# Kernel optimization log

Hardware: AMD Instinct MI355X
Metric: run time of the kernel (lower is better)

The kernel has to match this reference:

```python
import jax, jax.numpy as jnp
import numpy as np
import math

B, S, HID, H, WBAND = 2, 4096, 768, 12, 128
D = HID // H  # 64


def _band_qk(q, k, w):
    """q,k: [B,S,H,D] -> banded scores [B,S,H,2w+1] (offset d -> key pos i+d-w)."""
    b, s, h, d = q.shape
    nc = s // w
    kp = jnp.pad(k, ((0, 0), (w, w), (0, 0), (0, 0)))  # zero padding_value
    idx = (jnp.arange(nc) * w)[:, None] + jnp.arange(3 * w)[None, :]  # [nc,3w]
    kw = kp[:, idx]                                   # [B,nc,3w,H,D]
    qc = q.reshape(b, nc, w, h, d)
    scores = jnp.einsum('bcxhd,bcyhd->bchxy', qc, kw)  # [B,nc,H,w,3w]
    # extract diagonals: P[x,dd] = scores[x, x+dd] via flatten/skew trick
    flat = scores.reshape(b, nc, h, w * 3 * w)
    flat = jnp.pad(flat, ((0, 0), (0, 0), (0, 0), (0, w)))
    diag = flat.reshape(b, nc, h, w, 3 * w + 1)[..., : 2 * w + 1]
    return diag.transpose(0, 1, 3, 2, 4).reshape(b, s, h, 2 * w + 1)


def _band_pv(p, v, w):
    """p: [B,S,H,2w+1], v: [B,S,H,D] -> context [B,S,H,D]."""
    b, s, h, k = p.shape
    d = v.shape[-1]
    nc = s // w
    vp = jnp.pad(v, ((0, 0), (w, w), (0, 0), (0, 0)))
    idx = (jnp.arange(nc) * w)[:, None] + jnp.arange(3 * w)[None, :]
    vw = vp[:, idx]                                   # [B,nc,3w,H,D]
    pc = p.reshape(b, nc, w, h, k).transpose(0, 1, 3, 2, 4)  # [B,nc,H,w,2w+1]
    pc = jnp.pad(pc, ((0, 0), (0, 0), (0, 0), (0, 0), (0, w)))  # [..,w,3w+1]
    band = pc.reshape(b, nc, h, w * (3 * w + 1))[..., : w * 3 * w]
    band = band.reshape(b, nc, h, w, 3 * w)           # M[x, x+dd] = p[x,dd]
    ctx = jnp.einsum('bchxy,bcyhd->bcxhd', band, vw)  # [B,nc,w,H,D]
    return ctx.reshape(b, s, h, d)


def setup_inputs() -> dict:
    key = jax.random.key(0)
    ks = jax.random.split(key, 8)
    init = lambda k, shp: (jax.random.normal(k, shp, jnp.float32) * 0.02)
    return {
        'x': jax.random.normal(ks[0], (B, S, HID), jnp.float32),
        'Wq': init(ks[1], (HID, HID)), 'bq': jnp.zeros((HID,), jnp.float32),
        'Wk': init(ks[2], (HID, HID)), 'bk': jnp.zeros((HID,), jnp.float32),
        'Wv': init(ks[3], (HID, HID)), 'bv': jnp.zeros((HID,), jnp.float32),
        'Wd': init(ks[4], (H, D, HID)), 'bd': jnp.zeros((HID,), jnp.float32),
        'gamma': jnp.ones((HID,), jnp.float32),
        'beta': jnp.zeros((HID,), jnp.float32),
    }


def reference(x, Wq, bq, Wk, bk, Wv, bv, Wd, bd, gamma, beta):
    w = WBAND
    b, s, _ = x.shape
    q = (x @ Wq + bq).reshape(b, s, H, D) / math.sqrt(D)
    k = (x @ Wk + bk).reshape(b, s, H, D)
    v = (x @ Wv + bv).reshape(b, s, H, D)
    scores = _band_qk(q, k, w)                        # [B,S,H,2w+1]
    # mask_invalid_locations: key pos i + d - w must lie in [0, S)
    pos = jnp.arange(s)[:, None] + jnp.arange(2 * w + 1)[None, :] - w
    valid = (pos >= 0) & (pos < s)                    # [S,2w+1]
    scores = jnp.where(valid[None, :, None, :], scores, -1e9)
    probs = jax.nn.softmax(scores, axis=-1)           # float32 softmax
    ctx = _band_pv(probs, v, w)                       # [B,S,H,D]
    proj = jnp.einsum('bfnd,ndh->bfh', ctx, Wd) + bd  # output projection
    y = x + proj                                      # residual (dropout=0)
    mu = jnp.mean(y, axis=-1, keepdims=True)
    var = jnp.mean(jnp.square(y - mu), axis=-1, keepdims=True)
    out = (y - mu) / jnp.sqrt(var + 1e-12) * gamma + beta
    return out
```

## Files before the change

### kernel.cpp

```cpp
#include <hip/hip_runtime.h>
#include <math.h>

typedef unsigned short u16;
typedef __bf16 bf16x8 __attribute__((ext_vector_type(8)));
typedef float f32x4 __attribute__((ext_vector_type(4)));

constexpr int Bc   = 2;
constexpr int Sc   = 4096;
constexpr int HIDc = 768;
constexpr int Hc   = 12;
constexpr int Dc   = 64;
constexpr int Wc   = 128;
constexpr int Mc   = Bc * Sc;

constexpr int QT2  = 64;
constexpr int WIN  = QT2 + 2 * Wc;
constexpr int NCT  = WIN / 16;

#define VM_BAR(N) asm volatile("s_waitcnt vmcnt(" #N ")\n\ts_barrier" ::: "memory")
#define BAR()     asm volatile("s_barrier" ::: "memory")

static __device__ __forceinline__ void load_lds16(const void* g, void* l) {
    __builtin_amdgcn_global_load_lds(
        (const __attribute__((address_space(1))) void*)g,
        (__attribute__((address_space(3))) void*)l, 16, 0, 0);
}
static __device__ __forceinline__ u16 to_bf16(float f) {
    return __builtin_bit_cast(u16, (__bf16)f);
}

__global__ __launch_bounds__(256) void prep_x(const float* __restrict__ x,
                                              u16* __restrict__ xb,
                                              u16* __restrict__ zpad)
{
    int i = blockIdx.x * 256 + threadIdx.x;
    float4 v = ((const float4*)x)[i];
    ushort4 o;
    o.x = to_bf16(v.x); o.y = to_bf16(v.y);
    o.z = to_bf16(v.z); o.w = to_bf16(v.w);
    ((ushort4*)xb)[i] = o;
    if (blockIdx.x == 0 && threadIdx.x < 128)
        ((int4*)zpad)[threadIdx.x] = make_int4(0, 0, 0, 0);
}

__global__ __launch_bounds__(256) void prep_w(
    const float* __restrict__ Wq, const float* __restrict__ Wk,
    const float* __restrict__ Wv, const float* __restrict__ Wd,
    u16* __restrict__ wqt, u16* __restrict__ wkt,
    u16* __restrict__ wvt, u16* __restrict__ wdt)
{
    const int z = blockIdx.z;
    const float* W = z == 0 ? Wq : z == 1 ? Wk : z == 2 ? Wv : Wd;
    u16* T         = z == 0 ? wqt : z == 1 ? wkt : z == 2 ? wvt : wdt;

    __shared__ float t[32][33];
    const int bx = blockIdx.x * 32, by = blockIdx.y * 32;
    const int tx = threadIdx.x & 31, ty = threadIdx.x >> 5;
#pragma unroll
    for (int i = 0; i < 32; i += 8)
        t[ty + i][tx] = W[(size_t)(by + ty + i) * HIDc + bx + tx];
    __syncthreads();
#pragma unroll
    for (int i = 0; i < 32; i += 8)
        T[(size_t)(bx + ty + i) * HIDc + by + tx] = to_bf16(t[tx][ty + i]);
}

__device__ __forceinline__ void stage64(const u16* __restrict__ A,
                                        const u16* __restrict__ Bt,
                                        int m0, int n0, int k0,
                                        u16* As, u16* Bs, int soff)
{
#pragma unroll
    for (int i = 0; i < 4; ++i) {
        int off  = soff + i * 1024;
        int row  = off >> 7;
        int slot = (off >> 4) & 7;
        int seg  = slot ^ (row & 7);
        load_lds16(A  + (size_t)(m0 + row) * HIDc + k0 + seg * 8, (char*)As + off);
        load_lds16(Bt + (size_t)(n0 + row) * HIDc + k0 + seg * 8, (char*)Bs + off);
    }
}

template <int SWAP>
__device__ __forceinline__ void gemm128_core(
    const u16* __restrict__ A, const u16* __restrict__ Bt,
    int m0, int n0, u16* As, u16* Bs, f32x4 (&acc)[4][4])
{
    const int lane = threadIdx.x & 63, wid = threadIdx.x >> 6;
    const int c16 = lane & 15, g = lane >> 4;
    const int wm = (wid >> 1) * 64, wn = (wid & 1) * 64;
    const int soff = wid * 4096 + lane * 16;

    stage64(A, Bt, m0, n0, 0, As, Bs, soff);
    int cur = 0;
    for (int t = 0; t < 12; ++t) {
        if (t < 11) {
            stage64(A, Bt, m0, n0, (t + 1) * 64,
                    As + (cur ^ 1) * 8192, Bs + (cur ^ 1) * 8192, soff);
            VM_BAR(8);
        } else {
            VM_BAR(0);
        }
        const u16* Ab = As + cur * 8192;
        const u16* Bb = Bs + cur * 8192;
#pragma unroll
        for (int kk = 0; kk < 2; ++kk) {
            bf16x8 af[4], bfr[4];
#pragma unroll
            for (int tt = 0; tt < 4; ++tt) {
                int ar = wm + tt * 16 + c16;
                int a8 = (kk * 4 + g) ^ (ar & 7);
                af[tt] = *(const bf16x8*)(Ab + ar * 64 + a8 * 8);
                int br = wn + tt * 16 + c16;
                int b8 = (kk * 4 + g) ^ (br & 7);
                bfr[tt] = *(const bf16x8*)(Bb + br * 64 + b8 * 8);
            }
            __builtin_amdgcn_s_setprio(1);
#pragma unroll
            for (int mt = 0; mt < 4; ++mt)
#pragma unroll
                for (int nt = 0; nt < 4; ++nt)
                    acc[mt][nt] = SWAP
                        ? __builtin_amdgcn_mfma_f32_16x16x32_bf16(
                              bfr[nt], af[mt], acc[mt][nt], 0, 0, 0)
                        : __builtin_amdgcn_mfma_f32_16x16x32_bf16(
                              af[mt], bfr[nt], acc[mt][nt], 0, 0, 0);
            __builtin_amdgcn_s_setprio(0);
        }
        BAR();
        cur ^= 1;
    }
}

__global__ __launch_bounds__(256) void gemm_qk_mfma(
    const u16* __restrict__ xb,
    const u16* __restrict__ wqt, const u16* __restrict__ wkt,
    const float* __restrict__ bq, const float* __restrict__ bk,
    u16* __restrict__ qg, u16* __restrict__ kg)
{
    __shared__ u16 As[16384], Bs[16384];
    const int z = blockIdx.z;
    const u16* Bt     = z ? wkt : wqt;
    const float* bias = z ? bk : bq;
    const float scale = z ? 1.0f : 0.125f;
    u16* outp         = z ? kg : qg;

    const int m0 = blockIdx.x * 128, n0 = blockIdx.y * 128;
    f32x4 acc[4][4];
#pragma unroll
    for (int i = 0; i < 4; ++i)
#pragma unroll
        for (int j = 0; j < 4; ++j) acc[i][j] = (f32x4){0.f, 0.f, 0.f, 0.f};

    gemm128_core<1>(xb, Bt, m0, n0, As, Bs, acc);

    const int lane = threadIdx.x & 63, wid = threadIdx.x >> 6;
    const int c16 = lane & 15, g = lane >> 4;
    const int wm = (wid >> 1) * 64, wn = (wid & 1) * 64;

#pragma unroll
    for (int mt = 0; mt < 4; ++mt) {
        int m = m0 + wm + mt * 16 + c16;
        int b = m >> 12, s = m & (Sc - 1);
        size_t rowbase = (size_t)(b * Hc) * Sc * Dc + (size_t)s * Dc;
#pragma unroll
        for (int nt = 0; nt < 4; ++nt) {
            int nb = n0 + wn + nt * 16 + g * 4;
            int h = nb >> 6, d0 = nb & 63;
            float4 b4 = *(const float4*)&bias[nb];
            ushort4 pk;
            pk.x = to_bf16((acc[mt][nt][0] + b4.x) * scale);
            pk.y = to_bf16((acc[mt][nt][1] + b4.y) * scale);
            pk.z = to_bf16((acc[mt][nt][2] + b4.z) * scale);
            pk.w = to_bf16((acc[mt][nt][3] + b4.w) * scale);
            *(ushort4*)&outp[rowbase + (size_t)h * Sc * Dc + d0] = pk;
        }
    }
}

__global__ __launch_bounds__(256) void gemm_v_mfma(
    const u16* __restrict__ xb, const u16* __restrict__ wvt,
    const float* __restrict__ bv, u16* __restrict__ vtg)
{
    __shared__ u16 As[16384], Bs[16384];
    const int m0 = blockIdx.x * 128, n0 = blockIdx.y * 128;
    f32x4 acc[4][4];
#pragma unroll
    for (int i = 0; i < 4; ++i)
#pragma unroll
        for (int j = 0; j < 4; ++j) acc[i][j] = (f32x4){0.f, 0.f, 0.f, 0.f};

    gemm128_core<0>(xb, wvt, m0, n0, As, Bs, acc);

    const int lane = threadIdx.x & 63, wid = threadIdx.x >> 6;
    const int c16 = lane & 15, g = lane >> 4;
    const int wm = (wid >> 1) * 64, wn = (wid & 1) * 64;

#pragma unroll
    for (int nt = 0; nt < 4; ++nt) {
        int n = n0 + wn + nt * 16 + c16;
        int h = n >> 6, d = n & 63;
        float bn = bv[n];
#pragma unroll
        for (int mt = 0; mt < 4; ++mt) {
            int m = m0 + wm + mt * 16 + g * 4;
            int b = m >> 12, s = m & (Sc - 1);
            size_t base = ((size_t)(b * Hc + h)) * Sc * Dc + (size_t)d * Sc + s;
            ushort4 pk;
            pk.x = to_bf16(acc[mt][nt][0] + bn);
            pk.y = to_bf16(acc[mt][nt][1] + bn);
            pk.z = to_bf16(acc[mt][nt][2] + bn);
            pk.w = to_bf16(acc[mt][nt][3] + bn);
            *(ushort4*)&vtg[base] = pk;
        }
    }
}

__global__ __launch_bounds__(256) void gemm_proj_mfma(
    const u16* __restrict__ ctxb, const u16* __restrict__ wdt,
    const float* __restrict__ bd, const float* __restrict__ x,
    float* __restrict__ y)
{
    __shared__ u16 As[16384], Bs[16384];
    const int m0 = blockIdx.x * 128, n0 = blockIdx.y * 128;
    f32x4 acc[4][4];
#pragma unroll
    for (int i = 0; i < 4; ++i)
#pragma unroll
        for (int j = 0; j < 4; ++j) acc[i][j] = (f32x4){0.f, 0.f, 0.f, 0.f};

    gemm128_core<1>(ctxb, wdt, m0, n0, As, Bs, acc);

    const int lane = threadIdx.x & 63, wid = threadIdx.x >> 6;
    const int c16 = lane & 15, g = lane >> 4;
    const int wm = (wid >> 1) * 64, wn = (wid & 1) * 64;

#pragma unroll
    for (int mt = 0; mt < 4; ++mt) {
        int m = m0 + wm + mt * 16 + c16;
#pragma unroll
        for (int nt = 0; nt < 4; ++nt) {
            int nb = n0 + wn + nt * 16 + g * 4;
            float4 b4 = *(const float4*)&bd[nb];
            float4 x4 = *(const float4*)&x[(size_t)m * HIDc + nb];
            float4 o4;
            o4.x = acc[mt][nt][0] + b4.x + x4.x;
            o4.y = acc[mt][nt][1] + b4.y + x4.y;
            o4.z = acc[mt][nt][2] + b4.z + x4.z;
            o4.w = acc[mt][nt][3] + b4.w + x4.w;
            *(float4*)&y[(size_t)m * HIDc + nb] = o4;
        }
    }
}

__global__ __launch_bounds__(256) void band_attn_mfma(
    const u16* __restrict__ qg, const u16* __restrict__ kg,
    const u16* __restrict__ vtg, const u16* __restrict__ zpad,
    u16* __restrict__ ctxb)
{
    extern __shared__ u16 sm[];
    u16* kwin = sm;
    u16* vt   = sm + 20480;
    u16* pm   = sm;

    const int L = blockIdx.x;
    const int xcd = L & 7, tt = L >> 3;
    const int hb = xcd * 3 + (tt % 3);
    const int qc = tt / 3;
    const int h = hb % Hc, b = hb / Hc;

    const int s0 = qc * QT2;
    const int tid = threadIdx.x;
    const int lane = tid & 63, wid = tid >> 6;
    const int c16 = lane & 15, g = lane >> 4;
    const size_t hbase = ((size_t)(b * Hc + h)) * Sc * Dc;

    const u16* qp = &qg[hbase + (size_t)(s0 + wid * 16 + c16) * Dc + g * 8];
    bf16x8 qa0 = *(const bf16x8*)qp;
    bf16x8 qa1 = *(const bf16x8*)(qp + 32);

#pragma unroll
    for (int i = 0; i < 10; ++i) {
        int c   = i * 4 + wid;
        int row = c * 8 + (lane >> 3);
        int seg = (lane & 7) ^ (lane >> 3);
        int pos = s0 - Wc + row;
        const u16* src = (pos >= 0 && pos < Sc)
                       ? &kg[hbase + (size_t)pos * Dc + seg * 8] : zpad;
        load_lds16(src, (char*)kwin + c * 1024 + (lane & 63) * 16);
    }
#pragma unroll
    for (int i = 0; i < 10; ++i) {
        int c   = i * 4 + wid;
        int idx = c * 64 + lane;
        int d   = idx / 40;
        int p   = idx - d * 40;
        int seg = (p & 0x38) | ((p ^ d) & 7);
        int pos0 = s0 - Wc + seg * 8;
        const u16* src = (pos0 >= 0 && pos0 < Sc)
                       ? &vtg[hbase + (size_t)d * Sc + pos0] : zpad;
        load_lds16(src, (char*)vt + idx * 16);
    }

    VM_BAR(10);

    f32x4 acc[NCT];
#pragma unroll
    for (int ct = 0; ct < NCT; ++ct) acc[ct] = (f32x4){0.f, 0.f, 0.f, 0.f};
    __builtin_amdgcn_s_setprio(1);
#pragma unroll
    for (int ct = 0; ct < NCT; ++ct) {
        int row = ct * 16 + c16;
        const u16* kb = kwin + row * 64;
        bf16x8 kb0 = *(const bf16x8*)(kb + (g       ^ (row & 7)) * 8);
        bf16x8 kb1 = *(const bf16x8*)(kb + ((g + 4) ^ (row & 7)) * 8);
        acc[ct] = __builtin_amdgcn_mfma_f32_16x16x32_bf16(qa0, kb0, acc[ct], 0, 0, 0);
        acc[ct] = __builtin_amdgcn_mfma_f32_16x16x32_bf16(qa1, kb1, acc[ct], 0, 0, 0);
    }
    __builtin_amdgcn_s_setprio(0);

    float mrow[4] = {-3e38f, -3e38f, -3e38f, -3e38f};
#pragma unroll
    for (int ct = 0; ct < NCT; ++ct) {
#pragma unroll
        for (int r = 0; r < 4; ++r) {
            int rl  = wid * 16 + g * 4 + r;
            int j   = ct * 16 + c16;
            int pos = s0 - Wc + j;
            bool valid = (j >= rl) && (j <= rl + 2 * Wc) && (pos >= 0) && (pos < Sc);
            float v = valid ? acc[ct][r] : -3e38f;
            acc[ct][r] = v;
            mrow[r] = fmaxf(mrow[r], v);
        }
    }
#pragma unroll
    for (int r = 0; r < 4; ++r)
#pragma unroll
        for (int off = 1; off < 16; off <<= 1)
            mrow[r] = fmaxf(mrow[r], __shfl_xor(mrow[r], off));

    float srow[4] = {0.f, 0.f, 0.f, 0.f};
#pragma unroll
    for (int ct = 0; ct < NCT; ++ct)
#pragma unroll
        for (int r = 0; r < 4; ++r) {
            float e = __expf(acc[ct][r] - mrow[r]);
            acc[ct][r] = e;
            srow[r] += e;
        }
#pragma unroll
    for (int r = 0; r < 4; ++r)
#pragma unroll
        for (int off = 1; off < 16; off <<= 1)
            srow[r] += __shfl_xor(srow[r], off);

    VM_BAR(0);

#pragma unroll
    for (int ct = 0; ct < NCT; ++ct)
#pragma unroll
        for (int r = 0; r < 4; ++r) {
            int q   = wid * 16 + g * 4 + r;
            int col = ct * 16 + c16;
            int sl  = col >> 3;
            int ph  = (sl & 0x38) | ((sl ^ q ^ (q >> 3)) & 7);
            pm[q * 320 + ph * 8 + (col & 7)] = to_bf16(acc[ct][r]);
        }

    float sq0 = __shfl(srow[0], (c16 >> 2) << 4);
    float sq1 = __shfl(srow[1], (c16 >> 2) << 4);
    float sq2 = __shfl(srow[2], (c16 >> 2) << 4);
    float sq3 = __shfl(srow[3], (c16 >> 2) << 4);
    int rr = c16 & 3;
    float sq = rr == 0 ? sq0 : rr == 1 ? sq1 : rr == 2 ? sq2 : sq3;
    float invq = 1.f / sq;

    f32x4 o[4];
#pragma unroll
    for (int dt = 0; dt < 4; ++dt) o[dt] = (f32x4){0.f, 0.f, 0.f, 0.f};
    const int qrow = wid * 16 + c16;
    __builtin_amdgcn_s_setprio(1);
#pragma unroll
    for (int ks = 0; ks < 10; ++ks) {
        int sl = ks * 4 + g;
        int ph = (sl & 0x38) | ((sl ^ qrow ^ (qrow >> 3)) & 7);
        bf16x8 pa = *(const bf16x8*)(pm + qrow * 320 + ph * 8);
#pragma unroll
        for (int dt = 0; dt < 4; ++dt) {
            int d  = dt * 16 + c16;
            int pv = (sl & 0x38) | ((sl ^ d) & 7);
            bf16x8 vb = *(const bf16x8*)(vt + d * 320 + pv * 8);
            o[dt] = __builtin_amdgcn_mfma_f32_16x16x32_bf16(vb, pa, o[dt], 0, 0, 0);
        }
    }
    __builtin_amdgcn_s_setprio(0);

    const size_t crow = ((size_t)(b * Sc + s0 + wid * 16 + c16)) * HIDc + h * Dc;
#pragma unroll
    for (int dt = 0; dt < 4; ++dt) {
        ushort4 pk;
        pk.x = to_bf16(o[dt][0] * invq);
        pk.y = to_bf16(o[dt][1] * invq);
        pk.z = to_bf16(o[dt][2] * invq);
        pk.w = to_bf16(o[dt][3] * invq);
        *(ushort4*)&ctxb[crow + dt * 16 + g * 4] = pk;
    }
}

__global__ __launch_bounds__(256) void ln_kernel(
    const float* __restrict__ y,
    const float* __restrict__ gamma, const float* __restrict__ beta,
    float* __restrict__ out)
{
    const int m = blockIdx.x;
    const float* row = y + (size_t)m * HIDc;
    const int t = threadIdx.x;
    float v0 = row[t], v1 = row[t + 256], v2 = row[t + 512];
    float s = v0 + v1 + v2;
    __shared__ float red[4];
    const int lane = t & 63, wid = t >> 6;
#pragma unroll
    for (int o = 1; o < 64; o <<= 1) s += __shfl_xor(s, o);
    if (lane == 0) red[wid] = s;
    __syncthreads();
    const float mu = (red[0] + red[1] + red[2] + red[3]) * (1.f / HIDc);
    v0 -= mu; v1 -= mu; v2 -= mu;
    float s2 = v0 * v0 + v1 * v1 + v2 * v2;
#pragma unroll
    for (int o = 1; o < 64; o <<= 1) s2 += __shfl_xor(s2, o);
    __syncthreads();
    if (lane == 0) red[wid] = s2;
    __syncthreads();
    const float var = (red[0] + red[1] + red[2] + red[3]) * (1.f / HIDc);
    const float rstd = rsqrtf(var + 1e-12f);
    const size_t base = (size_t)m * HIDc;
    out[base + t]       = v0 * rstd * gamma[t]       + beta[t];
    out[base + t + 256] = v1 * rstd * gamma[t + 256] + beta[t + 256];
    out[base + t + 512] = v2 * rstd * gamma[t + 512] + beta[t + 512];
}

extern "C" void kernel_launch(void* const* d_in, const int* in_sizes, int n_in,
                              void* d_out, int out_size, void* d_ws, size_t ws_size,
                              hipStream_t stream)
{
    const float* x     = (const float*)d_in[0];
    const float* Wq    = (const float*)d_in[1];
    const float* bq    = (const float*)d_in[2];
    const float* Wk    = (const float*)d_in[3];
    const float* bk    = (const float*)d_in[4];
    const float* Wv    = (const float*)d_in[5];
    const float* bv    = (const float*)d_in[6];
    const float* Wd    = (const float*)d_in[7];
    const float* bd    = (const float*)d_in[8];
    const float* gamma = (const float*)d_in[9];
    const float* beta  = (const float*)d_in[10];
    float* out = (float*)d_out;

    constexpr size_t CHUNK = (size_t)Mc * HIDc;
    constexpr size_t WSZ   = (size_t)HIDc * HIDc;
    u16* xb   = (u16*)d_ws;
    u16* wqt  = xb + CHUNK;
    u16* wkt  = wqt + WSZ;
    u16* wvt  = wkt + WSZ;
    u16* wdt  = wvt + WSZ;
    u16* qg   = wdt + WSZ;
    u16* kg   = qg + CHUNK;
    u16* vtg  = kg + CHUNK;
    u16* ctxb = vtg + CHUNK;
    float* yws = (float*)(ctxb + CHUNK);
    u16* zpad  = (u16*)(yws + CHUNK);

    prep_x<<<(CHUNK / 4) / 256, 256, 0, stream>>>(x, xb, zpad);
    prep_w<<<dim3(24, 24, 4), 256, 0, stream>>>(Wq, Wk, Wv, Wd, wqt, wkt, wvt, wdt);

    gemm_qk_mfma<<<dim3(Mc / 128, HIDc / 128, 2), 256, 0, stream>>>(
        xb, wqt, wkt, bq, bk, qg, kg);
    gemm_v_mfma<<<dim3(Mc / 128, HIDc / 128), 256, 0, stream>>>(
        xb, wvt, bv, vtg);

    band_attn_mfma<<<dim3(Sc / QT2 * Hc * Bc), 256, 81920, stream>>>(
        qg, kg, vtg, zpad, ctxb);

    gemm_proj_mfma<<<dim3(Mc / 128, HIDc / 128), 256, 0, stream>>>(
        ctxb, wdt, bd, x, yws);

    ln_kernel<<<Mc, 256, 0, stream>>>(yws, gamma, beta, out);
}
```

Measured before the change: 126.7 us.

## Widen band attention to 128-query tiles with per-wave diagonal key windows

The band-attention kernel now runs 512-thread blocks over 128 queries. The K/V window grows to 384 keys, so loaded K/V is shared by twice as many queries and there are half as many blocks. Each wave computes only the 18 key tiles its 16 rows can reach rather than the whole window, which cuts wasted QK and PV MFMA work on masked entries. The probability staging buffer shrinks to 192 columns and is filled and consumed in two halves. The cost is larger LDS use per block (96 KB), more registers per wave and fewer blocks, which may lower occupancy.

```diff
diff --git a/kernel.cpp b/kernel.cpp
--- a/kernel.cpp
+++ b/kernel.cpp
@@ -13,9 +13,9 @@
 constexpr int Wc   = 128;
 constexpr int Mc   = Bc * Sc;
 
-constexpr int QT2  = 64;
-constexpr int WIN  = QT2 + 2 * Wc;
-constexpr int NCT  = WIN / 16;
+constexpr int QT3  = 128;
+constexpr int WIN3 = 384;
+constexpr int NCT3 = 18;
 
 #define VM_BAR(N) asm volatile("s_waitcnt vmcnt(" #N ")\n\ts_barrier" ::: "memory")
 #define BAR()     asm volatile("s_barrier" ::: "memory")
@@ -253,14 +253,14 @@
     }
 }
 
-__global__ __launch_bounds__(256) void band_attn_mfma(
+__global__ __launch_bounds__(512) void band_attn_mfma(
     const u16* __restrict__ qg, const u16* __restrict__ kg,
     const u16* __restrict__ vtg, const u16* __restrict__ zpad,
     u16* __restrict__ ctxb)
 {
     extern __shared__ u16 sm[];
     u16* kwin = sm;
-    u16* vt   = sm + 20480;
+    u16* vt   = sm + 24576;
     u16* pm   = sm;
 
     const int L = blockIdx.x;
@@ -269,19 +269,19 @@
     const int qc = tt / 3;
     const int h = hb % Hc, b = hb / Hc;
 
-    const int s0 = qc * QT2;
+    const int s0 = qc * QT3;
     const int tid = threadIdx.x;
-    const int lane = tid & 63, wid = tid >> 6;
+    const int lane = tid & 63, w = tid >> 6;
     const int c16 = lane & 15, g = lane >> 4;
     const size_t hbase = ((size_t)(b * Hc + h)) * Sc * Dc;
 
-    const u16* qp = &qg[hbase + (size_t)(s0 + wid * 16 + c16) * Dc + g * 8];
+    const u16* qp = &qg[hbase + (size_t)(s0 + w * 16 + c16) * Dc + g * 8];
     bf16x8 qa0 = *(const bf16x8*)qp;
     bf16x8 qa1 = *(const bf16x8*)(qp + 32);
 
 #pragma unroll
-    for (int i = 0; i < 10; ++i) {
-        int c   = i * 4 + wid;
+    for (int i = 0; i < 6; ++i) {
+        int c   = i * 8 + w;
         int row = c * 8 + (lane >> 3);
         int seg = (lane & 7) ^ (lane >> 3);
         int pos = s0 - Wc + row;
@@ -290,27 +290,29 @@
         load_lds16(src, (char*)kwin + c * 1024 + (lane & 63) * 16);
     }
 #pragma unroll
-    for (int i = 0; i < 10; ++i) {
-        int c   = i * 4 + wid;
+    for (int i = 0; i < 6; ++i) {
+        int c   = i * 8 + w;
         int idx = c * 64 + lane;
-        int d   = idx / 40;
-        int p   = idx - d * 40;
-        int seg = (p & 0x38) | ((p ^ d) & 7);
+        int d   = idx / 48;
+        int p   = idx - d * 48;
+        int seg = (p & ~7) | ((p ^ d) & 7);
         int pos0 = s0 - Wc + seg * 8;
         const u16* src = (pos0 >= 0 && pos0 < Sc)
                        ? &vtg[hbase + (size_t)d * Sc + pos0] : zpad;
         load_lds16(src, (char*)vt + idx * 16);
     }
 
-    VM_BAR(10);
-
-    f32x4 acc[NCT];
-#pragma unroll
-    for (int ct = 0; ct < NCT; ++ct) acc[ct] = (f32x4){0.f, 0.f, 0.f, 0.f};
+    VM_BAR(6);
+
+    const int tb  = w & ~1;
+    const int off = (w & 1) * 16;
+    f32x4 acc[NCT3];
+#pragma unroll
+    for (int ct = 0; ct < NCT3; ++ct) acc[ct] = (f32x4){0.f, 0.f, 0.f, 0.f};
     __builtin_amdgcn_s_setprio(1);
 #pragma unroll
-    for (int ct = 0; ct < NCT; ++ct) {
-        int row = ct * 16 + c16;
+    for (int ct = 0; ct < NCT3; ++ct) {
+        int row = (tb + ct) * 16 + c16;
         const u16* kb = kwin + row * 64;
         bf16x8 kb0 = *(const bf16x8*)(kb + (g       ^ (row & 7)) * 8);
         bf16x8 kb1 = *(const bf16x8*)(kb + ((g + 4) ^ (row & 7)) * 8);
@@ -321,13 +323,13 @@
 
     float mrow[4] = {-3e38f, -3e38f, -3e38f, -3e38f};
 #pragma unroll
-    for (int ct = 0; ct < NCT; ++ct) {
+    for (int ct = 0; ct < NCT3; ++ct) {
 #pragma unroll
         for (int r = 0; r < 4; ++r) {
-            int rl  = wid * 16 + g * 4 + r;
-            int j   = ct * 16 + c16;
-            int pos = s0 - Wc + j;
-            bool valid = (j >= rl) && (j <= rl + 2 * Wc) && (pos >= 0) && (pos < Sc);
+            int ql  = g * 4 + r;
+            int jl  = ct * 16 + c16 - off;
+            int pos = s0 - Wc + (tb + ct) * 16 + c16;
+            bool valid = (jl >= ql) && (jl <= ql + 2 * Wc) && (pos >= 0) && (pos < Sc);
             float v = valid ? acc[ct][r] : -3e38f;
             acc[ct][r] = v;
             mrow[r] = fmaxf(mrow[r], v);
@@ -336,12 +338,12 @@
 #pragma unroll
     for (int r = 0; r < 4; ++r)
 #pragma unroll
-        for (int off = 1; off < 16; off <<= 1)
-            mrow[r] = fmaxf(mrow[r], __shfl_xor(mrow[r], off));
+        for (int o2 = 1; o2 < 16; o2 <<= 1)
+            mrow[r] = fmaxf(mrow[r], __shfl_xor(mrow[r], o2));
 
     float srow[4] = {0.f, 0.f, 0.f, 0.f};
 #pragma unroll
-    for (int ct = 0; ct < NCT; ++ct)
+    for (int ct = 0; ct < NCT3; ++ct)
 #pragma unroll
         for (int r = 0; r < 4; ++r) {
             float e = __expf(acc[ct][r] - mrow[r]);
@@ -351,21 +353,10 @@
 #pragma unroll
     for (int r = 0; r < 4; ++r)
 #pragma unroll
-        for (int off = 1; off < 16; off <<= 1)
-            srow[r] += __shfl_xor(srow[r], off);
+        for (int o2 = 1; o2 < 16; o2 <<= 1)
+            srow[r] += __shfl_xor(srow[r], o2);
 
     VM_BAR(0);
-
-#pragma unroll
-    for (int ct = 0; ct < NCT; ++ct)
-#pragma unroll
-        for (int r = 0; r < 4; ++r) {
-            int q   = wid * 16 + g * 4 + r;
-            int col = ct * 16 + c16;
-            int sl  = col >> 3;
-            int ph  = (sl & 0x38) | ((sl ^ q ^ (q >> 3)) & 7);
-            pm[q * 320 + ph * 8 + (col & 7)] = to_bf16(acc[ct][r]);
-        }
 
     float sq0 = __shfl(srow[0], (c16 >> 2) << 4);
     float sq1 = __shfl(srow[1], (c16 >> 2) << 4);
@@ -375,27 +366,66 @@
     float sq = rr == 0 ? sq0 : rr == 1 ? sq1 : rr == 2 ? sq2 : sq3;
     float invq = 1.f / sq;
 
+    const int qrow = w * 16 + c16;
     f32x4 o[4];
 #pragma unroll
     for (int dt = 0; dt < 4; ++dt) o[dt] = (f32x4){0.f, 0.f, 0.f, 0.f};
-    const int qrow = wid * 16 + c16;
+
+#pragma unroll
+    for (int ct = 0; ct < 10; ++ct)
+#pragma unroll
+        for (int r = 0; r < 4; ++r) {
+            int q   = w * 16 + g * 4 + r;
+            int col = ct * 16 + c16;
+            int sl  = col >> 3;
+            int ph  = (sl & ~7) | ((sl ^ q ^ (q >> 3)) & 7);
+            pm[q * 192 + ph * 8 + (col & 7)] = to_bf16(acc[ct][r]);
+        }
     __builtin_amdgcn_s_setprio(1);
 #pragma unroll
-    for (int ks = 0; ks < 10; ++ks) {
+    for (int ks = 0; ks < 5; ++ks) {
         int sl = ks * 4 + g;
-        int ph = (sl & 0x38) | ((sl ^ qrow ^ (qrow >> 3)) & 7);
-        bf16x8 pa = *(const bf16x8*)(pm + qrow * 320 + ph * 8);
+        int ph = (sl & ~7) | ((sl ^ qrow ^ (qrow >> 3)) & 7);
+        bf16x8 pa = *(const bf16x8*)(pm + qrow * 192 + ph * 8);
 #pragma unroll
         for (int dt = 0; dt < 4; ++dt) {
             int d  = dt * 16 + c16;
-            int pv = (sl & 0x38) | ((sl ^ d) & 7);
-            bf16x8 vb = *(const bf16x8*)(vt + d * 320 + pv * 8);
+            int vs = tb * 2 + ks * 4 + g;
+            int pv = (vs & ~7) | ((vs ^ d) & 7);
+            bf16x8 vb = *(const bf16x8*)(vt + d * 384 + pv * 8);
             o[dt] = __builtin_amdgcn_mfma_f32_16x16x32_bf16(vb, pa, o[dt], 0, 0, 0);
         }
     }
     __builtin_amdgcn_s_setprio(0);
 
-    const size_t crow = ((size_t)(b * Sc + s0 + wid * 16 + c16)) * HIDc + h * Dc;
+#pragma unroll
+    for (int ct = 10; ct < NCT3; ++ct)
+#pragma unroll
+        for (int r = 0; r < 4; ++r) {
+            int q   = w * 16 + g * 4 + r;
+            int col = ct * 16 + c16 - 160;
+            int sl  = col >> 3;
+            int ph  = (sl & ~7) | ((sl ^ q ^ (q >> 3)) & 7);
+            pm[q * 192 + ph * 8 + (col & 7)] = to_bf16(acc[ct][r]);
+        }
+    __builtin_amdgcn_s_setprio(1);
+#pragma unroll
+    for (int ks = 0; ks < 4; ++ks) {
+        int sl = ks * 4 + g;
+        int ph = (sl & ~7) | ((sl ^ qrow ^ (qrow >> 3)) & 7);
+        bf16x8 pa = *(const bf16x8*)(pm + qrow * 192 + ph * 8);
+#pragma unroll
+        for (int dt = 0; dt < 4; ++dt) {
+            int d  = dt * 16 + c16;
+            int vs = tb * 2 + 20 + ks * 4 + g;
+            int pv = (vs & ~7) | ((vs ^ d) & 7);
+            bf16x8 vb = *(const bf16x8*)(vt + d * 384 + pv * 8);
+            o[dt] = __builtin_amdgcn_mfma_f32_16x16x32_bf16(vb, pa, o[dt], 0, 0, 0);
+        }
+    }
+    __builtin_amdgcn_s_setprio(0);
+
+    const size_t crow = ((size_t)(b * Sc + s0 + qrow)) * HIDc + h * Dc;
 #pragma unroll
     for (int dt = 0; dt < 4; ++dt) {
         ushort4 pk;
@@ -478,7 +508,7 @@
     gemm_v_mfma<<<dim3(Mc / 128, HIDc / 128), 256, 0, stream>>>(
         xb, wvt, bv, vtg);
 
-    band_attn_mfma<<<dim3(Sc / QT2 * Hc * Bc), 256, 81920, stream>>>(
+    band_attn_mfma<<<dim3(Sc / QT3 * Hc * Bc), 512, 98304, stream>>>(
         qg, kg, vtg, zpad, ctxb);
 
     gemm_proj_mfma<<<dim3(Mc / 128, HIDc / 128), 256, 0, stream>>>(
```

Result: no change. 127.2 us (+0.4%).
